# Performance work log

Measured on AMD Instinct MI355X. Metric: run time of the kernel, lower is better.

The kernel has to match this reference:

```python
import jax, jax.numpy as jnp
import numpy as np

SIGMA = 1.0
DELTA = 1.0
TOPK = 10
TOPK_HALF = int(np.around(TOPK / 2))  # 5
EPS = 1e-12


def _cdist(a, b):
    # Euclidean distance matrix, grad-safe sqrt at zero (matches torch.cdist values).
    d2 = (jnp.sum(a * a, axis=1)[:, None]
          + jnp.sum(b * b, axis=1)[None, :]
          - 2.0 * (a @ b.T))
    d2 = jnp.maximum(d2, 0.0)
    pos = d2 > 0.0
    return jnp.where(pos, jnp.sqrt(jnp.where(pos, d2, 1.0)), 0.0)


def _consistency_weights(t_emb):
    # Everything here is under torch.no_grad() in the original.
    N = t_emb.shape[0]
    T_dist = _cdist(t_emb, t_emb)
    W_P = jnp.exp(-(T_dist ** 2) / SIGMA)
    _, idx = jax.lax.top_k(W_P, TOPK)                      # [N, TOPK]
    rows = jnp.arange(N)[:, None]
    W_NN = jnp.zeros_like(W_P).at[rows, idx].set(1.0)      # scatter_ ones
    V = (((W_NN + W_NN.T) / 2) == 1.0).astype(W_P.dtype)   # mutual kNN (symmetric)
    # Vectorized form of the per-row python loop:
    #   W_C_tilda[i, j] = V[i, j] * (sum_k V[i, k] * V[j, k]) / sum_k V[i, k]
    deg = jnp.sum(V, axis=1)                               # >= 1 (self is always a NN)
    overlap = V @ V.T                                      # [N, N] neighbor overlap
    W_C_tilda = V * overlap / deg[:, None]
    topk_half_index = idx[:, :TOPK_HALF]                   # [N, TOPK_HALF]
    W_C_hat = jnp.mean(W_C_tilda[topk_half_index], axis=1) # gather rows, mean -> [N, N]
    W_C = (W_C_hat + W_C_hat.T) / 2
    return (W_P + W_C) / 2


def reference(s_emb, t_emb):
    # disable_mu = 0 -> s_emb NOT normalized; t_emb always normalized.
    t_norm = t_emb / jnp.maximum(
        jnp.linalg.norm(t_emb, axis=1, keepdims=True), EPS)
    N = s_emb.shape[0]
    S_dist = _cdist(s_emb, s_emb)
    S_dist = S_dist / jnp.mean(S_dist, axis=1, keepdims=True)
    W = jax.lax.stop_gradient(_consistency_weights(t_norm))
    off_diag = 1.0 - jnp.eye(N, dtype=W.dtype)
    pos_weight = W * off_diag
    neg_weight = (1.0 - W) * off_diag
    pull = jnp.maximum(S_dist, 0.0) ** 2 * pos_weight
    push = jnp.maximum(DELTA - S_dist, 0.0) ** 2 * neg_weight
    return (jnp.sum(pull) + jnp.sum(push)) / (N * (N - 1))


def setup_inputs() -> dict:
    key = jax.random.key(0)
    k1, k2 = jax.random.split(key)
    N, D = 2048, 1024
    return {
        "s_emb": jax.random.normal(k1, (N, D), dtype=jnp.float32),
        "t_emb": jax.random.normal(k2, (N, D), dtype=jnp.float32),
    }
```

## Files before the change

### kernel.cpp

```cpp
#include <hip/hip_runtime.h>
#include <math.h>

#define N_ 2048
#define D_ 1024
#define TOPK 10
#define TOPK_HALF 5
#define NTRI 528
#define INV_NORM (1.0f / ((float)N_ * (float)(N_ - 1)))

typedef __attribute__((ext_vector_type(8))) short short8;
typedef __attribute__((ext_vector_type(16))) float floatx16;

__device__ __forceinline__ short f2bf(float f) {
  unsigned u = __float_as_uint(f);
  unsigned r = (u + 0x7fffu + ((u >> 16) & 1u)) >> 16;
  return (short)r;
}
__device__ __forceinline__ float bf2f(short b) {
  return __uint_as_float(((unsigned)(unsigned short)b) << 16);
}

__device__ __forceinline__ void gld_lds16(const short* g, short* l) {
  __builtin_amdgcn_global_load_lds(
      (const __attribute__((address_space(1))) unsigned int*)(g),
      (__attribute__((address_space(3))) unsigned int*)(l), 16, 0, 0);
}

#define BAR() asm volatile("s_barrier" ::: "memory")
#define WAIT4_BAR() asm volatile("s_waitcnt vmcnt(4)\ns_barrier" ::: "memory")
#define WAIT0_BAR() asm volatile("s_waitcnt vmcnt(0)\ns_barrier" ::: "memory")

__global__ __launch_bounds__(256) void prep_kernel(const float* __restrict__ t,
                                                   const float* __restrict__ s,
                                                   short* __restrict__ tb,
                                                   short* __restrict__ sb,
                                                   float* __restrict__ tt,
                                                   float* __restrict__ ss,
                                                   float* __restrict__ rowsum,
                                                   float* __restrict__ out) {
  int b = blockIdx.x, tid = threadIdx.x;
  __shared__ float red[256];
  if (b == 0) {
    for (int j = tid; j < N_; j += 256) rowsum[j] = 0.f;
    if (tid == 0) out[0] = 0.f;
  }
  if (b < N_) {
    const float4* rp = (const float4*)(t + (size_t)b * D_);
    float4 v = rp[tid];
    red[tid] = v.x * v.x + v.y * v.y + v.z * v.z + v.w * v.w;
    __syncthreads();
    for (int st = 128; st > 0; st >>= 1) { if (tid < st) red[tid] += red[tid + st]; __syncthreads(); }
    float inv = 1.f / fmaxf(sqrtf(red[0]), 1e-12f);
    __syncthreads();
    float a = v.x * inv, bb = v.y * inv, c = v.z * inv, d = v.w * inv;
    uint2 pk;
    pk.x = (unsigned)(unsigned short)f2bf(a) | ((unsigned)(unsigned short)f2bf(bb) << 16);
    pk.y = (unsigned)(unsigned short)f2bf(c) | ((unsigned)(unsigned short)f2bf(d) << 16);
    ((uint2*)(tb + (size_t)b * D_))[tid] = pk;
    red[tid] = a * a + bb * bb + c * c + d * d;
    __syncthreads();
    for (int st = 128; st > 0; st >>= 1) { if (tid < st) red[tid] += red[tid + st]; __syncthreads(); }
    if (tid == 0) tt[b] = red[0];
  } else {
    int row = b - N_;
    const float4* rp = (const float4*)(s + (size_t)row * D_);
    float4 v = rp[tid];
    uint2 pk;
    pk.x = (unsigned)(unsigned short)f2bf(v.x) | ((unsigned)(unsigned short)f2bf(v.y) << 16);
    pk.y = (unsigned)(unsigned short)f2bf(v.z) | ((unsigned)(unsigned short)f2bf(v.w) << 16);
    ((uint2*)(sb + (size_t)row * D_))[tid] = pk;
    red[tid] = v.x * v.x + v.y * v.y + v.z * v.z + v.w * v.w;
    __syncthreads();
    for (int st = 128; st > 0; st >>= 1) { if (tid < st) red[tid] += red[tid + st]; __syncthreads(); }
    if (tid == 0) ss[row] = red[0];
  }
}

__global__ __launch_bounds__(256) void gram_sym_kernel(
    const short* __restrict__ Tb, const short* __restrict__ Sb,
    const float* __restrict__ tt, const float* __restrict__ ss,
    short* __restrict__ WPb, short* __restrict__ Sob,
    float* __restrict__ rowsum) {
  int p = blockIdx.x;
  const int mode = (p >= NTRI);
  int q = p - mode * NTRI;
  int bi = (int)((sqrtf(8.f * (float)q + 1.f) - 1.f) * 0.5f);
  if (bi > 31) bi = 31;
  while ((bi + 1) * (bi + 2) / 2 <= q) bi++;
  while (bi * (bi + 1) / 2 > q) bi--;
  int bj = q - bi * (bi + 1) / 2;

  const short* A = mode ? Sb : Tb;
  const float* rn = mode ? ss : tt;
  short* outb = mode ? Sob : WPb;

  __shared__ __align__(16) short smem[4 * 4096];

  int tid = threadIdx.x;
  int w = tid >> 6, lane = tid & 63;
  int i0 = bi * 64, j0 = bj * 64;
  int wr = w >> 1, wc = w & 1;
  int l32 = lane & 31, half = lane >> 5;

  floatx16 acc = {};

  int sr8 = lane >> 3;
  int gch = ((lane & 7) ^ sr8) * 8;
  const short* Ag = A + (size_t)(i0 + w * 16 + sr8) * D_ + gch;
  const short* Bg = A + (size_t)(j0 + w * 16 + sr8) * D_ + gch;
  int lloc = (w * 16 + sr8) * 64 + (lane & 7) * 8;

#define STAGE(buf, k0)                                       \
  do {                                                       \
    short* Al = smem + (buf)*8192 + lloc;                    \
    short* Bl = smem + (buf)*8192 + 4096 + lloc;             \
    gld_lds16(Ag + (k0), Al);                                \
    gld_lds16(Ag + (k0) + (size_t)8 * D_, Al + 512);         \
    gld_lds16(Bg + (k0), Bl);                                \
    gld_lds16(Bg + (k0) + (size_t)8 * D_, Bl + 512);         \
  } while (0)

  STAGE(0, 0);
#pragma unroll 2
  for (int it = 0; it < 16; it++) {
    int cur = it & 1;
    if (it) BAR();
    if (it < 15) {
      STAGE(!cur, (it + 1) * 64);
      WAIT4_BAR();
    } else {
      WAIT0_BAR();
    }
    const short* Ab = smem + cur * 8192;
    const short* Bb = smem + cur * 8192 + 4096;
#pragma unroll
    for (int kstep = 0; kstep < 4; kstep++) {
      int cA = (((2 * kstep + half) ^ (l32 & 7)) << 3);
      short8 af = *(const short8*)&Ab[(wr * 32 + l32) * 64 + cA];
      short8 bfr = *(const short8*)&Bb[(wc * 32 + l32) * 64 + cA];
      acc = __builtin_amdgcn_mfma_f32_32x32x16_bf16(af, bfr, acc, 0, 0, 0);
    }
  }

  float ov[16];
  int jcol = j0 + wc * 32 + l32;
  float rj = rn[jcol];
#pragma unroll
  for (int reg = 0; reg < 16; reg++) {
    int rl = (reg & 3) + 8 * (reg >> 2) + 4 * half;
    int i = i0 + wr * 32 + rl;
    float d2 = fmaxf(rn[i] + rj - 2.f * acc[reg], 0.f);
    float o = mode ? sqrtf(d2) : expf(-d2);
    if (i == jcol) o = mode ? 0.f : 1.f;
    ov[reg] = o;
    outb[(size_t)i * N_ + jcol] = f2bf(o);
  }
  if (mode) {
#pragma unroll
    for (int reg = 0; reg < 16; reg++) {
      float rs = ov[reg];
      rs += __shfl_xor(rs, 1); rs += __shfl_xor(rs, 2);
      rs += __shfl_xor(rs, 4); rs += __shfl_xor(rs, 8);
      rs += __shfl_xor(rs, 16);
      if (l32 == 0) {
        int rl = (reg & 3) + 8 * (reg >> 2) + 4 * half;
        atomicAdd(&rowsum[i0 + wr * 32 + rl], rs);
      }
    }
  }

  if (bi != bj) {
    if (mode) {
      float cs = 0.f;
#pragma unroll
      for (int reg = 0; reg < 16; reg++) cs += ov[reg];
      cs += __shfl_xor(cs, 32);
      if (half == 0) atomicAdd(&rowsum[jcol], cs);
    }
    BAR();
    float* fs = (float*)smem + w * 1088;
#pragma unroll
    for (int reg = 0; reg < 16; reg++) {
      int rl = (reg & 3) + 8 * (reg >> 2) + 4 * half;
      fs[l32 * 34 + rl] = ov[reg];
    }
#pragma unroll
    for (int itx = 0; itx < 8; itx++) {
      int sidx = itx * 64 + lane;
      int lc = sidx >> 4;
      int k2 = (sidx & 15) * 2;
      float lo = fs[lc * 34 + k2];
      float hi = fs[lc * 34 + k2 + 1];
      unsigned pk = (unsigned)(unsigned short)f2bf(lo) |
                    ((unsigned)(unsigned short)f2bf(hi) << 16);
      size_t jg = (size_t)(j0 + wc * 32 + lc);
      *(unsigned*)(outb + jg * N_ + i0 + wr * 32 + k2) = pk;
    }
  }
}

__global__ __launch_bounds__(64) void topk_loss_kernel(const short* __restrict__ WPb,
                                                       const short* __restrict__ Sb,
                                                       const float* __restrict__ rowsum,
                                                       int* __restrict__ idx,
                                                       float* __restrict__ out) {
  int row = blockIdx.x, lane = threadIdx.x;
  const short8* wpr = (const short8*)(WPb + (size_t)row * N_);
  const short8* sr = (const short8*)(Sb + (size_t)row * N_);
  float rminv = (float)N_ / rowsum[row];
  float w[32];
  float local = 0.f;
#pragma unroll
  for (int c4 = 0; c4 < 4; c4++) {
    short8 wp8 = wpr[lane * 4 + c4];
    short8 s8 = sr[lane * 4 + c4];
#pragma unroll
    for (int e = 0; e < 8; e++) {
      float wv = bf2f(wp8[e]);
      w[c4 * 8 + e] = wv;
      float sv = bf2f(s8[e]) * rminv;
      float d = fmaxf(1.f - sv, 0.f);
      local += d * d + 0.5f * wv * (sv * sv - d * d);
    }
  }
#pragma unroll
  for (int off = 32; off > 0; off >>= 1) local += __shfl_down(local, off);
  if (lane == 0) atomicAdd(out, (local - 0.5f) * INV_NORM);
  int base = lane * 32;
  int sel[TOPK];
  for (int t = 0; t < TOPK; t++) {
    float bv = -2.f; int bi = 0;
#pragma unroll
    for (int c = 0; c < 32; c++)
      if (w[c] > bv) { bv = w[c]; bi = base + c; }
#pragma unroll
    for (int off = 32; off > 0; off >>= 1) {
      float ovv = __shfl_down(bv, off);
      int oi = __shfl_down(bi, off);
      if (ovv > bv || (ovv == bv && oi < bi)) { bv = ovv; bi = oi; }
    }
    bi = __shfl(bi, 0);
    sel[t] = bi;
    bool mine = (bi >> 5) == lane;
    int cc = bi & 31;
#pragma unroll
    for (int c = 0; c < 32; c++)
      if (mine && cc == c) w[c] = -1.f;
  }
  if (lane == 0) {
#pragma unroll
    for (int t = 0; t < TOPK; t++) idx[row * TOPK + t] = sel[t];
  }
}

__device__ __forceinline__ unsigned mutual_mask(const int* __restrict__ idx, int x) {
  unsigned m = 0;
  int nb[TOPK];
#pragma unroll
  for (int k = 0; k < TOPK; k++) nb[k] = idx[x * TOPK + k];
#pragma unroll
  for (int k = 0; k < TOPK; k++) {
    int j = nb[k];
    bool mut = false;
#pragma unroll
    for (int l = 0; l < TOPK; l++) mut |= (idx[j * TOPK + l] == x);
    if (mut) m |= 1u << k;
  }
  return m;
}

__global__ __launch_bounds__(256) void sparse_wc_kernel(
    const int* __restrict__ idx, const short* __restrict__ Sb,
    const float* __restrict__ rowsum, float* __restrict__ out) {
  int t = blockIdx.x * 256 + threadIdx.x;
  int i = t >> 6, r = t & 63;
  float contrib = 0.f;
  if (i < N_ && r < TOPK_HALF * TOPK) {
    int mi = r / TOPK, k = r - mi * TOPK;
    int m = idx[i * TOPK + mi];
    unsigned mm = mutual_mask(idx, m);
    if ((mm >> k) & 1u) {
      int col = idx[m * TOPK + k];
      if (col != i) {
        int dm = __popc(mm);
        unsigned mc = mutual_mask(idx, col);
        int jm[TOPK], jc[TOPK];
#pragma unroll
        for (int l = 0; l < TOPK; l++) jm[l] = idx[m * TOPK + l];
#pragma unroll
        for (int l = 0; l < TOPK; l++) jc[l] = idx[col * TOPK + l];
        int c = 0;
#pragma unroll
        for (int a = 0; a < TOPK; a++) {
          if ((mm >> a) & 1u) {
            int na = jm[a];
#pragma unroll
            for (int b = 0; b < TOPK; b++) c += (((mc >> b) & 1u) && (jc[b] == na));
          }
        }
        float v = (float)c / (float)dm * 0.1f;
        float s1 = bf2f(Sb[(size_t)i * N_ + col]) * ((float)N_ / rowsum[i]);
        float d1 = fmaxf(1.f - s1, 0.f);
        float s2 = bf2f(Sb[(size_t)col * N_ + i]) * ((float)N_ / rowsum[col]);
        float d2 = fmaxf(1.f - s2, 0.f);
        contrib = 0.5f * v * ((s1 * s1 - d1 * d1) + (s2 * s2 - d2 * d2));
      }
    }
  }
  __shared__ float red[256];
  red[threadIdx.x] = contrib; __syncthreads();
  for (int st = 128; st > 0; st >>= 1) {
    if (threadIdx.x < st) red[threadIdx.x] += red[threadIdx.x + st];
    __syncthreads();
  }
  if (threadIdx.x == 0) atomicAdd(out, red[0] * INV_NORM);
}

extern "C" void kernel_launch(void* const* d_in, const int* in_sizes, int n_in,
                              void* d_out, int out_size, void* d_ws, size_t ws_size,
                              hipStream_t stream) {
  const float* s_emb = (const float*)d_in[0];
  const float* t_emb = (const float*)d_in[1];
  float* out = (float*)d_out;

  const size_t NN = (size_t)N_ * N_;
  const size_t ND = (size_t)N_ * D_;
  short* t_bf = (short*)d_ws;
  short* s_bf = t_bf + ND;
  short* WPb = s_bf + ND;
  short* Sb = WPb + NN;
  float* tt = (float*)(Sb + NN);
  float* ss = tt + N_;
  float* rowsum = ss + N_;
  int* idx = (int*)(rowsum + N_);

  prep_kernel<<<2 * N_, 256, 0, stream>>>(t_emb, s_emb, t_bf, s_bf, tt, ss, rowsum, out);

  gram_sym_kernel<<<2 * NTRI, 256, 0, stream>>>(t_bf, s_bf, tt, ss, WPb, Sb, rowsum);

  topk_loss_kernel<<<N_, 64, 0, stream>>>(WPb, Sb, rowsum, idx, out);
  sparse_wc_kernel<<<N_ * 64 / 256, 256, 0, stream>>>(idx, Sb, rowsum, out);
}
```

Before: 151.2 us.

## Deepen gram kernel LDS pipeline to four stages and precompute mutual-kNN masks

The Gram kernel's global-to-LDS staging goes from double buffering to a four-buffer ring with three tiles in flight, and the wait counts are adjusted per iteration. This is meant to hide more memory latency. LDS per block rises to 64 KB, which may lower occupancy. Separately, the mutual-kNN bitmask per row is now computed once in a new small kernel using atomicOr, instead of being recomputed twice per thread in sparse_wc_kernel. That trades repeated index loads for one extra kernel launch.

```diff
diff --git a/kernel.cpp b/kernel.cpp
--- a/kernel.cpp
+++ b/kernel.cpp
@@ -27,6 +27,8 @@
 }
 
 #define BAR() asm volatile("s_barrier" ::: "memory")
+#define WAIT12_BAR() asm volatile("s_waitcnt vmcnt(12)\ns_barrier" ::: "memory")
+#define WAIT8_BAR() asm volatile("s_waitcnt vmcnt(8)\ns_barrier" ::: "memory")
 #define WAIT4_BAR() asm volatile("s_waitcnt vmcnt(4)\ns_barrier" ::: "memory")
 #define WAIT0_BAR() asm volatile("s_waitcnt vmcnt(0)\ns_barrier" ::: "memory")
 
@@ -94,7 +96,7 @@
   const float* rn = mode ? ss : tt;
   short* outb = mode ? Sob : WPb;
 
-  __shared__ __align__(16) short smem[4 * 4096];
+  __shared__ __align__(16) short smem[4 * 8192];
 
   int tid = threadIdx.x;
   int w = tid >> 6, lane = tid & 63;
@@ -121,18 +123,18 @@
   } while (0)
 
   STAGE(0, 0);
-#pragma unroll 2
+  STAGE(1, 64);
+  STAGE(2, 128);
+#pragma unroll
   for (int it = 0; it < 16; it++) {
-    int cur = it & 1;
     if (it) BAR();
-    if (it < 15) {
-      STAGE(!cur, (it + 1) * 64);
-      WAIT4_BAR();
-    } else {
-      WAIT0_BAR();
-    }
-    const short* Ab = smem + cur * 8192;
-    const short* Bb = smem + cur * 8192 + 4096;
+    if (it + 3 < 16) STAGE((it + 3) & 3, (it + 3) * 64);
+    if (it < 13) WAIT12_BAR();
+    else if (it == 13) WAIT8_BAR();
+    else if (it == 14) WAIT4_BAR();
+    else WAIT0_BAR();
+    const short* Ab = smem + (it & 3) * 8192;
+    const short* Bb = smem + (it & 3) * 8192 + 4096;
 #pragma unroll
     for (int kstep = 0; kstep < 4; kstep++) {
       int cA = (((2 * kstep + half) ^ (l32 & 7)) << 3);
@@ -203,6 +205,7 @@
                                                        const short* __restrict__ Sb,
                                                        const float* __restrict__ rowsum,
                                                        int* __restrict__ idx,
+                                                       unsigned* __restrict__ mask,
                                                        float* __restrict__ out) {
   int row = blockIdx.x, lane = threadIdx.x;
   const short8* wpr = (const short8*)(WPb + (size_t)row * N_);
@@ -225,7 +228,10 @@
   }
 #pragma unroll
   for (int off = 32; off > 0; off >>= 1) local += __shfl_down(local, off);
-  if (lane == 0) atomicAdd(out, (local - 0.5f) * INV_NORM);
+  if (lane == 0) {
+    atomicAdd(out, (local - 0.5f) * INV_NORM);
+    mask[row] = 0u;
+  }
   int base = lane * 32;
   int sel[TOPK];
   for (int t = 0; t < TOPK; t++) {
@@ -253,37 +259,34 @@
   }
 }
 
-__device__ __forceinline__ unsigned mutual_mask(const int* __restrict__ idx, int x) {
-  unsigned m = 0;
-  int nb[TOPK];
-#pragma unroll
-  for (int k = 0; k < TOPK; k++) nb[k] = idx[x * TOPK + k];
-#pragma unroll
-  for (int k = 0; k < TOPK; k++) {
-    int j = nb[k];
-    bool mut = false;
-#pragma unroll
-    for (int l = 0; l < TOPK; l++) mut |= (idx[j * TOPK + l] == x);
-    if (mut) m |= 1u << k;
-  }
-  return m;
+__global__ __launch_bounds__(256) void mutual_kernel(const int* __restrict__ idx,
+                                                     unsigned* __restrict__ mask) {
+  int t = blockIdx.x * 256 + threadIdx.x;
+  int i = t >> 4, k = t & 15;
+  if (i >= N_ || k >= TOPK) return;
+  int j = idx[i * TOPK + k];
+  bool mut = false;
+#pragma unroll
+  for (int l = 0; l < TOPK; l++) mut |= (idx[j * TOPK + l] == i);
+  if (mut) atomicOr(&mask[i], 1u << k);
 }
 
 __global__ __launch_bounds__(256) void sparse_wc_kernel(
-    const int* __restrict__ idx, const short* __restrict__ Sb,
-    const float* __restrict__ rowsum, float* __restrict__ out) {
+    const int* __restrict__ idx, const unsigned* __restrict__ mask,
+    const short* __restrict__ Sb, const float* __restrict__ rowsum,
+    float* __restrict__ out) {
   int t = blockIdx.x * 256 + threadIdx.x;
   int i = t >> 6, r = t & 63;
   float contrib = 0.f;
   if (i < N_ && r < TOPK_HALF * TOPK) {
     int mi = r / TOPK, k = r - mi * TOPK;
     int m = idx[i * TOPK + mi];
-    unsigned mm = mutual_mask(idx, m);
+    unsigned mm = mask[m];
     if ((mm >> k) & 1u) {
       int col = idx[m * TOPK + k];
       if (col != i) {
         int dm = __popc(mm);
-        unsigned mc = mutual_mask(idx, col);
+        unsigned mc = mask[col];
         int jm[TOPK], jc[TOPK];
 #pragma unroll
         for (int l = 0; l < TOPK; l++) jm[l] = idx[m * TOPK + l];
@@ -333,11 +336,13 @@
   float* ss = tt + N_;
   float* rowsum = ss + N_;
   int* idx = (int*)(rowsum + N_);
+  unsigned* mask = (unsigned*)(idx + (size_t)N_ * TOPK);
 
   prep_kernel<<<2 * N_, 256, 0, stream>>>(t_emb, s_emb, t_bf, s_bf, tt, ss, rowsum, out);
 
   gram_sym_kernel<<<2 * NTRI, 256, 0, stream>>>(t_bf, s_bf, tt, ss, WPb, Sb, rowsum);
 
-  topk_loss_kernel<<<N_, 64, 0, stream>>>(WPb, Sb, rowsum, idx, out);
-  sparse_wc_kernel<<<N_ * 64 / 256, 256, 0, stream>>>(idx, Sb, rowsum, out);
-}
+  topk_loss_kernel<<<N_, 64, 0, stream>>>(WPb, Sb, rowsum, idx, mask, out);
+  mutual_kernel<<<N_ * 16 / 256, 256, 0, stream>>>(idx, mask);
+  sparse_wc_kernel<<<N_ * 64 / 256, 256, 0, stream>>>(idx, mask, Sb, rowsum, out);
+}
```

Result: slower. 158.6 us (+4.9%).
